# Kernel tuning notes

Measured on AMD Instinct MI355X. Metric: run time of the kernel, lower is better.

The kernel has to match this reference:

```python
import jax, jax.numpy as jnp
import numpy as np

B, C, H, W = 16, 256, 32, 32   # batch, codebook_dim (channels), latent grid
K = 16384                      # codebook_size
BETA = 0.25                    # commitment beta


def setup_inputs() -> dict:
    key = jax.random.key(0)
    k1, k2, k3 = jax.random.split(key, 3)
    x = jax.random.normal(k1, (B, C, H, W), dtype=jnp.float32)
    # binary-ish mask, broadcast over channel dim (c=1)
    codebook_mask = (jax.random.uniform(k2, (B, 1, H, W)) < 0.5).astype(jnp.float32)
    # uniform(-1/K, 1/K) init as in the torch module
    weight = jax.random.uniform(k3, (K, C), dtype=jnp.float32,
                                minval=-1.0 / K, maxval=1.0 / K)
    return {"x": x, "codebook_mask": codebook_mask, "weight": weight}


def reference(x, codebook_mask, weight):
    b, c, h, w = x.shape
    n = h * w
    # b c h w -> b (h w) c
    xf = jnp.transpose(x, (0, 2, 3, 1)).reshape(b, n, c)
    mask = jnp.transpose(codebook_mask, (0, 2, 3, 1)).reshape(b, n, 1)

    flat = xf.reshape(b * n, c)
    # negative squared euclidean distance: -|f|^2 - |w|^2 + 2 f.w
    dist = (-jnp.sum(flat * flat, axis=1, keepdims=True)
            - jnp.sum(weight * weight, axis=1)
            + 2.0 * flat @ weight.T)                      # [b*n, K]
    # temp=0 -> gumbel_sample degenerates to argmax
    embed_ind = jnp.argmax(dist, axis=-1).reshape(b, n)    # int indices
    x_q = weight[embed_ind]                                # [b, n, c] gather

    # masked commitment loss
    ratio = 1.0 / jnp.mean(mask)
    loss = (ratio * BETA * jnp.mean((jax.lax.stop_gradient(x_q) - xf) ** 2 * mask)
            + ratio * jnp.mean((x_q - jax.lax.stop_gradient(xf)) ** 2 * mask))

    # straight-through estimator
    x_q_st = xf + jax.lax.stop_gradient(x_q - xf)

    x_q_img = jnp.transpose(x_q_st.reshape(b, h, w, c), (0, 3, 1, 2))
    embed_ind_img = embed_ind.reshape(b, h, w)
    return x_q_img, loss, embed_ind_img
```

## Files before the change

kernel.cpp:

```cpp
#include <hip/hip_runtime.h>

#define KCODES 16384
#define NPOS   16384
#define KQUART 4096
#define ROWS   64
#define CAPH   80
#define M_INT  5700
#define SX     21.166666f
#define SW     2080768.0f

#define OFF_XT    0
#define OFF_XQ8   4194304
#define OFF_PART  6291456
#define OFF_WHP8  8388608
#define OFF_CAND  9437184
#define OFF_WN    12582912
#define OFF_NS1   12599296
#define OFF_IDX   12615680
#define OFF_CCNT  12632064
#define OFF_QMAX  12697600

#define OUT_LOSS  4194304
#define OUT_IND   4194305

#define AS1 __attribute__((address_space(1)))
#define AS3 __attribute__((address_space(3)))

typedef int  i32x4 __attribute__((ext_vector_type(4)));

__global__ void k1a_pack_x(const float* __restrict__ x, float* __restrict__ xt)
{
    __shared__ float t[32][33];
    const int p0 = blockIdx.x * 32, c0 = blockIdx.y * 32, b = blockIdx.z;
    const int tx = threadIdx.x, ty = threadIdx.y;
#pragma unroll
    for (int i = 0; i < 4; ++i) {
        int cl = ty + i * 8;
        t[cl][tx] = x[(b * 256 + c0 + cl) * 1024 + p0 + tx];
    }
    __syncthreads();
#pragma unroll
    for (int i = 0; i < 4; ++i) {
        int pl = ty + i * 8;
        xt[(b * 1024 + p0 + pl) * 256 + c0 + tx] = t[tx][pl];
    }
}

__global__ void k_rownorm2(const float4* __restrict__ xt4, float* __restrict__ ns1,
                           signed char* __restrict__ xq8,
                           const float4* __restrict__ w4, float* __restrict__ wn,
                           signed char* __restrict__ wq8)
{
    __shared__ float4 rows[32 * 64];
    const int tid = threadIdx.x;
    const bool wpath = blockIdx.x >= 512;
    const int r0 = (wpath ? blockIdx.x - 512 : blockIdx.x) * 32;
    const float4* __restrict__ src4 = wpath ? w4 : xt4;
    float* __restrict__ out = wpath ? wn : ns1;
    const float sign = wpath ? 1.0f : -1.0f;
    const float sc = wpath ? SW : SX;
#pragma unroll
    for (int i = 0; i < 8; ++i) {
        const int F = r0 * 64 + tid + 256 * i;
        const float4 v = src4[F];
        rows[tid + 256 * i] = v;
        char4 qv;
        qv.x = (signed char)min(127, max(-127, __float2int_rn(v.x * sc)));
        qv.y = (signed char)min(127, max(-127, __float2int_rn(v.y * sc)));
        qv.z = (signed char)min(127, max(-127, __float2int_rn(v.z * sc)));
        qv.w = (signed char)min(127, max(-127, __float2int_rn(v.w * sc)));
        const int row = F >> 6, c4 = F & 63, c = c4 * 4;
        if (wpath) {
            const int qt = row >> 12, kk = row & 4095;
            const int chi = kk >> 8, rem = kk & 255;
            const int wq_ = rem >> 6, ct = (rem >> 4) & 3, n4 = rem & 15;
            const int sidx = qt * 1048576 + (chi * 4 + (c >> 6)) * 16384
                           + wq_ * 4096 + ct * 1024 + n4 * 64 + (c & 63);
            *(char4*)(wq8 + sidx) = qv;
        } else {
            *(char4*)(xq8 + row * 256 + c) = qv;
        }
    }
    __syncthreads();
    const int rl = tid >> 3, j = tid & 7;
    const float* qp = (const float*)&rows[rl * 64];
    float h[2];
#pragma unroll
    for (int half = 0; half < 2; ++half) {
        const float* p = qp + half * 128;
        float x = p[j];
        float r = __fmul_rn(x, x);
#pragma unroll
        for (int i = 1; i < 16; ++i) {
            float y = p[8 * i + j];
            r = __fadd_rn(r, __fmul_rn(y, y));
        }
        float t = __fadd_rn(r, __shfl_xor(r, 1));
        t = __fadd_rn(t, __shfl_xor(t, 2));
        t = __fadd_rn(t, __shfl_xor(t, 4));
        h[half] = t;
    }
    if (j == 0) out[r0 + rl] = sign * __fadd_rn(h[0], h[1]);
}

__global__ __launch_bounds__(256, 4) void k2_mfma(
    const signed char* __restrict__ xq8, const signed char* __restrict__ wq8,
    unsigned short* __restrict__ candk, int* __restrict__ candc,
    float* __restrict__ qmax)
{
    __shared__ __align__(16) signed char As[16384];
    __shared__ int rowmaxI[ROWS];
    __shared__ int ccnt[ROWS];
    __shared__ unsigned short ck[ROWS][CAPH];

    const int tid  = threadIdx.x;
    const int lane = tid & 63;
    const int w    = tid >> 6;
    const int q    = lane >> 4;
    const int nn   = lane & 15;
    const int qt   = blockIdx.x & 3;
    const int rowBase = (blockIdx.x >> 2) * ROWS;
    const signed char* wq8Q = wq8 + qt * 1048576;

#pragma unroll
    for (int i = 0; i < 4; ++i) {
        const int slot = i * 256 + tid;
        const int g = slot >> 6, row = slot & 63;
        const signed char* src = xq8 + (rowBase + row) * 256 + g * 16;
        __builtin_amdgcn_global_load_lds((const AS1 void*)src,
                                         (AS3 void*)((char*)&As[0] + slot * 16), 16, 0, 0);
    }
    if (tid < ROWS) { rowmaxI[tid] = (int)0x80000000; ccnt[tid] = 0; }

    const signed char* bptr = wq8Q + (w * 4096 + nn * 64 + q * 16);

    __syncthreads();

    i32x4 b0[4], b1[4];
#pragma unroll
    for (int ct = 0; ct < 4; ++ct)
        b0[ct] = *(const i32x4*)(bptr + ct * 1024);
    const signed char* nps = bptr + 16384;

    for (int ch = 0; ch < 16; ++ch) {
        const int kb = ch * 256;
        i32x4 acc[4][4];
#pragma unroll
        for (int rt = 0; rt < 4; ++rt)
#pragma unroll
            for (int ct = 0; ct < 4; ++ct) acc[rt][ct] = (i32x4){0, 0, 0, 0};

#pragma unroll
        for (int cs2 = 0; cs2 < 2; ++cs2) {
#pragma unroll
            for (int ct = 0; ct < 4; ++ct)
                b1[ct] = *(const i32x4*)(nps + ct * 1024);
            nps += 16384;
#pragma unroll
            for (int rt = 0; rt < 4; ++rt) {
                const int as = ((2 * cs2) * 4 + q) * 64 + rt * 16 + nn;
                const i32x4 ah = *(const i32x4*)&As[as * 16];
#pragma unroll
                for (int ct = 0; ct < 4; ++ct)
                    acc[rt][ct] = __builtin_amdgcn_mfma_i32_16x16x64_i8(ah, b0[ct], acc[rt][ct], 0, 0, 0);
            }
#pragma unroll
            for (int ct = 0; ct < 4; ++ct)
                b0[ct] = *(const i32x4*)(nps + ct * 1024);
            nps += 16384;
#pragma unroll
            for (int rt = 0; rt < 4; ++rt) {
                const int as = ((2 * cs2 + 1) * 4 + q) * 64 + rt * 16 + nn;
                const i32x4 ah = *(const i32x4*)&As[as * 16];
#pragma unroll
                for (int ct = 0; ct < 4; ++ct)
                    acc[rt][ct] = __builtin_amdgcn_mfma_i32_16x16x64_i8(ah, b1[ct], acc[rt][ct], 0, 0, 0);
            }
        }

#pragma unroll
        for (int rt = 0; rt < 4; ++rt)
#pragma unroll
            for (int rg = 0; rg < 4; ++rg) {
                int m = max(max(acc[rt][0][rg], acc[rt][1][rg]),
                            max(acc[rt][2][rg], acc[rt][3][rg]));
                m = max(m, __shfl_xor(m, 1, 64));
                m = max(m, __shfl_xor(m, 2, 64));
                m = max(m, __shfl_xor(m, 4, 64));
                m = max(m, __shfl_xor(m, 8, 64));
                if (nn == 0)
                    atomicMax(&rowmaxI[rt * 16 + q * 4 + rg], m);
            }
        __syncthreads();
#pragma unroll
        for (int rt = 0; rt < 4; ++rt)
#pragma unroll
            for (int rg = 0; rg < 4; ++rg) {
                const int row = rt * 16 + q * 4 + rg;
                const int th = rowmaxI[row] - M_INT;
#pragma unroll
                for (int ct = 0; ct < 4; ++ct)
                    if (acc[rt][ct][rg] >= th) {
                        const int pos = atomicAdd(&ccnt[row], 1);
                        if (pos < CAPH)
                            ck[row][pos] = (unsigned short)(qt * KQUART + kb + w * 64 + ct * 16 + nn);
                    }
            }
    }
    __syncthreads();
    if (tid < ROWS) {
        candc[(rowBase + tid) * 4 + qt] = ccnt[tid];
        qmax[(rowBase + tid) * 4 + qt] = (float)rowmaxI[tid];
    }
#pragma unroll
    for (int i = 0; i < 20; ++i) {
        const int e = i * 256 + tid;
        const int row = e / CAPH, pos = e - row * CAPH;
        candk[((rowBase + row) * 4 + qt) * CAPH + pos] = ck[row][pos];
    }
}

__global__ __launch_bounds__(256) void k3_rescore(
    const float* __restrict__ xt, const float* __restrict__ weight,
    const float* __restrict__ wn, const float* __restrict__ ns1,
    const float* __restrict__ qmax,
    const unsigned short* __restrict__ candk, const int* __restrict__ candc,
    const float* __restrict__ mask,
    int* __restrict__ idx, float* __restrict__ out, float* __restrict__ part)
{
    const int w = threadIdx.x >> 6, lane = threadIdx.x & 63;
    const int waveId = blockIdx.x * 4 + w;
    float mm = 0.f, merr = 0.f;
#pragma unroll
    for (int rr = 0; rr < 4; ++rr) {
        const int n = waveId * 4 + rr;
        const float4 xv = ((const float4*)(xt + n * 256))[lane];
        const float nsv = ns1[n];
        const float4 qm = ((const float4*)(qmax + n * 4))[0];
        const float qth = fmaxf(fmaxf(qm.x, qm.y), fmaxf(qm.z, qm.w)) - (float)M_INT;
        float bestd = -3.0e38f; int bestk = 0x7fffffff;
#pragma unroll
        for (int qt = 0; qt < 4; ++qt) {
            const float qv = (qt == 0) ? qm.x : (qt == 1) ? qm.y : (qt == 2) ? qm.z : qm.w;
            if (qv < qth) continue;
            const int cnt = candc[n * 4 + qt];
            if (cnt <= CAPH) {
                for (int i = 0; i < cnt; ++i) {
                    const int k = candk[(n * 4 + qt) * CAPH + i];
                    const float4 wv = ((const float4*)(weight + k * 256))[lane];
                    float p = __fmul_rn(xv.x, wv.x);
                    p = __builtin_fmaf(xv.y, wv.y, p);
                    p = __builtin_fmaf(xv.z, wv.z, p);
                    p = __builtin_fmaf(xv.w, wv.w, p);
#pragma unroll
                    for (int off = 1; off < 64; off <<= 1) p += __shfl_xor(p, off, 64);
                    const float t1 = __fadd_rn(nsv, -wn[k]);
                    const float dd = __fadd_rn(t1, __fmul_rn(2.0f, p));
                    if (dd > bestd || (dd == bestd && k < bestk)) { bestd = dd; bestk = k; }
                }
            } else {
                for (int k = qt * KQUART; k < (qt + 1) * KQUART; ++k) {
                    const float4 wv = ((const float4*)(weight + k * 256))[lane];
                    float p = __fmul_rn(xv.x, wv.x);
                    p = __builtin_fmaf(xv.y, wv.y, p);
                    p = __builtin_fmaf(xv.z, wv.z, p);
                    p = __builtin_fmaf(xv.w, wv.w, p);
#pragma unroll
                    for (int off = 1; off < 64; off <<= 1) p += __shfl_xor(p, off, 64);
                    const float t1 = __fadd_rn(nsv, -wn[k]);
                    const float dd = __fadd_rn(t1, __fmul_rn(2.0f, p));
                    if (dd > bestd || (dd == bestd && k < bestk)) { bestd = dd; bestk = k; }
                }
            }
        }
        const int bk = (bestk <= (KCODES - 1)) ? bestk : 0;
        if (lane == 0) { idx[n] = bk; out[OUT_IND + n] = (float)bk; }
        const float4 wv = ((const float4*)(weight + bk * 256))[lane];
        float ex = wv.x - xv.x, ey = wv.y - xv.y, ez = wv.z - xv.z, ew = wv.w - xv.w;
        float s = ex * ex + ey * ey + ez * ez + ew * ew;
#pragma unroll
        for (int off = 1; off < 64; off <<= 1) s += __shfl_xor(s, off, 64);
        const float mval = mask[n];
        mm += mval; merr += mval * s;
    }
    if (lane == 0) { part[waveId * 2 + 0] = mm; part[waveId * 2 + 1] = merr; }
}

__global__ void k5_out(const float* __restrict__ weight, const int* __restrict__ idx,
                       const float* __restrict__ part, float* __restrict__ out)
{
    __shared__ float t[32][33];
    const int p0 = blockIdx.x * 32, c0 = blockIdx.y * 32, b = blockIdx.z;
    const int tx = threadIdx.x, ty = threadIdx.y;
#pragma unroll
    for (int i = 0; i < 4; ++i) {
        const int pl = ty + i * 8;
        const int n = b * 1024 + p0 + pl;
        t[tx][pl] = weight[idx[n] * 256 + c0 + tx];
    }
    __syncthreads();
#pragma unroll
    for (int i = 0; i < 4; ++i) {
        const int cl = ty + i * 8;
        out[(b * 256 + c0 + cl) * 1024 + p0 + tx] = t[cl][tx];
    }
    if (blockIdx.x == 0 && blockIdx.y == 0 && blockIdx.z == 0) {
        __shared__ double red[4][2];
        const int lin = ty * 32 + tx;
        double m = 0.0, s = 0.0;
        for (int i = lin; i < 4096; i += 256) {
            m += (double)part[i * 2 + 0];
            s += (double)part[i * 2 + 1];
        }
        const int lane = lin & 63, wv = lin >> 6;
        for (int o = 32; o > 0; o >>= 1) {
            m += __shfl_down(m, o, 64);
            s += __shfl_down(s, o, 64);
        }
        if (lane == 0) { red[wv][0] = m; red[wv][1] = s; }
        __syncthreads();
        if (lin == 0) {
            const double mt = red[0][0] + red[1][0] + red[2][0] + red[3][0];
            const double st = red[0][1] + red[1][1] + red[2][1] + red[3][1];
            out[OUT_LOSS] = (float)(1.25 * st / (256.0 * mt));
        }
    }
}

extern "C" void kernel_launch(void* const* d_in, const int* in_sizes, int n_in,
                              void* d_out, int out_size, void* d_ws, size_t ws_size,
                              hipStream_t stream)
{
    const float* x      = (const float*)d_in[0];
    const float* mask   = (const float*)d_in[1];
    const float* weight = (const float*)d_in[2];
    float* out = (float*)d_out;
    float* ws  = (float*)d_ws;

    float* xt  = ws + OFF_XT;
    signed char* xq8 = (signed char*)(ws + OFF_XQ8);
    signed char* wq8 = (signed char*)(ws + OFF_WHP8);
    float* wn   = ws + OFF_WN;
    float* ns1  = ws + OFF_NS1;
    int*   idx  = (int*)(ws + OFF_IDX);
    unsigned short* candk = (unsigned short*)(ws + OFF_CAND);
    int*   candc = (int*)(ws + OFF_CCNT);
    float* qmaxA = ws + OFF_QMAX;
    float* part = ws + OFF_PART;

    k1a_pack_x<<<dim3(32, 8, 16), dim3(32, 8), 0, stream>>>(x, xt);
    k_rownorm2<<<1024, 256, 0, stream>>>((const float4*)xt, ns1, xq8,
                                         (const float4*)weight, wn, wq8);
    k2_mfma<<<1024, 256, 0, stream>>>(xq8, wq8, candk, candc, qmaxA);
    k3_rescore<<<1024, 256, 0, stream>>>(xt, weight, wn, ns1, qmaxA, candk, candc,
                                         mask, idx, out, part);
    k5_out<<<dim3(32, 8, 16), dim3(32, 8), 0, stream>>>(weight, idx, part, out);
}
```

Baseline: 295.1 us.

## Fuse transpose into prep kernel, tighten rescore margin, pair candidate rescoring

Merges the x transpose kernel and the row-norm/quantize kernel into one launch, so the transposed rows go straight from shared memory to xt, xq8 and the norms without re-reading xt. Lowers the int8 quarter-pruning margin M_INT so fewer codebook quarters get rescored in fp32. Unrolls the candidate rescoring loop two at a time so two weight loads and their reductions can overlap. The smaller margin risks picking a different argmax when int8 quantization error exceeds the new bound.

```diff
diff --git a/kernel.cpp b/kernel.cpp
--- a/kernel.cpp
+++ b/kernel.cpp
@@ -5,7 +5,7 @@
 #define KQUART 4096
 #define ROWS   64
 #define CAPH   80
-#define M_INT  5700
+#define M_INT  3600
 #define SX     21.166666f
 #define SW     2080768.0f
 
@@ -28,79 +28,110 @@
 
 typedef int  i32x4 __attribute__((ext_vector_type(4)));
 
-__global__ void k1a_pack_x(const float* __restrict__ x, float* __restrict__ xt)
+__global__ void k_prep(const float* __restrict__ x, float* __restrict__ xt,
+                       signed char* __restrict__ xq8, float* __restrict__ ns1,
+                       const float4* __restrict__ w4, float* __restrict__ wn,
+                       signed char* __restrict__ wq8)
 {
+    __shared__ __align__(16) float smem[32 * 257];
     __shared__ float t[32][33];
-    const int p0 = blockIdx.x * 32, c0 = blockIdx.y * 32, b = blockIdx.z;
-    const int tx = threadIdx.x, ty = threadIdx.y;
-#pragma unroll
-    for (int i = 0; i < 4; ++i) {
-        int cl = ty + i * 8;
-        t[cl][tx] = x[(b * 256 + c0 + cl) * 1024 + p0 + tx];
-    }
-    __syncthreads();
-#pragma unroll
-    for (int i = 0; i < 4; ++i) {
-        int pl = ty + i * 8;
-        xt[(b * 1024 + p0 + pl) * 256 + c0 + tx] = t[tx][pl];
-    }
-}
-
-__global__ void k_rownorm2(const float4* __restrict__ xt4, float* __restrict__ ns1,
-                           signed char* __restrict__ xq8,
-                           const float4* __restrict__ w4, float* __restrict__ wn,
-                           signed char* __restrict__ wq8)
-{
-    __shared__ float4 rows[32 * 64];
     const int tid = threadIdx.x;
-    const bool wpath = blockIdx.x >= 512;
-    const int r0 = (wpath ? blockIdx.x - 512 : blockIdx.x) * 32;
-    const float4* __restrict__ src4 = wpath ? w4 : xt4;
-    float* __restrict__ out = wpath ? wn : ns1;
-    const float sign = wpath ? 1.0f : -1.0f;
-    const float sc = wpath ? SW : SX;
-#pragma unroll
-    for (int i = 0; i < 8; ++i) {
-        const int F = r0 * 64 + tid + 256 * i;
-        const float4 v = src4[F];
-        rows[tid + 256 * i] = v;
-        char4 qv;
-        qv.x = (signed char)min(127, max(-127, __float2int_rn(v.x * sc)));
-        qv.y = (signed char)min(127, max(-127, __float2int_rn(v.y * sc)));
-        qv.z = (signed char)min(127, max(-127, __float2int_rn(v.z * sc)));
-        qv.w = (signed char)min(127, max(-127, __float2int_rn(v.w * sc)));
-        const int row = F >> 6, c4 = F & 63, c = c4 * 4;
-        if (wpath) {
+
+    if (blockIdx.x < 512) {
+        const int r0 = blockIdx.x * 32;
+        const int b = r0 >> 10, p0 = r0 & 1023;
+        const int tx = tid & 31, ty = tid >> 5;
+#pragma unroll
+        for (int ci = 0; ci < 8; ++ci) {
+#pragma unroll
+            for (int i = 0; i < 4; ++i) {
+                const int cl = ty + i * 8;
+                t[cl][tx] = x[(b * 256 + ci * 32 + cl) * 1024 + p0 + tx];
+            }
+            __syncthreads();
+#pragma unroll
+            for (int i = 0; i < 4; ++i) {
+                const int pl = ty + i * 8;
+                smem[pl * 257 + ci * 32 + tx] = t[tx][pl];
+            }
+            __syncthreads();
+        }
+#pragma unroll
+        for (int i = 0; i < 8; ++i) {
+            const int row = (tid >> 6) + i * 4, c4 = tid & 63;
+            const float* rp = &smem[row * 257 + c4 * 4];
+            float4 v;
+            v.x = rp[0]; v.y = rp[1]; v.z = rp[2]; v.w = rp[3];
+            ((float4*)(xt + (r0 + row) * 256))[c4] = v;
+            char4 qv;
+            qv.x = (signed char)min(127, max(-127, __float2int_rn(v.x * SX)));
+            qv.y = (signed char)min(127, max(-127, __float2int_rn(v.y * SX)));
+            qv.z = (signed char)min(127, max(-127, __float2int_rn(v.z * SX)));
+            qv.w = (signed char)min(127, max(-127, __float2int_rn(v.w * SX)));
+            *(char4*)(xq8 + (r0 + row) * 256 + c4 * 4) = qv;
+        }
+        __syncthreads();
+        const int rl = tid >> 3, j = tid & 7;
+        const float* qp = &smem[rl * 257];
+        float h[2];
+#pragma unroll
+        for (int half = 0; half < 2; ++half) {
+            const float* p = qp + half * 128;
+            float xx = p[j];
+            float r = __fmul_rn(xx, xx);
+#pragma unroll
+            for (int i = 1; i < 16; ++i) {
+                float y = p[8 * i + j];
+                r = __fadd_rn(r, __fmul_rn(y, y));
+            }
+            float tt = __fadd_rn(r, __shfl_xor(r, 1));
+            tt = __fadd_rn(tt, __shfl_xor(tt, 2));
+            tt = __fadd_rn(tt, __shfl_xor(tt, 4));
+            h[half] = tt;
+        }
+        if (j == 0) ns1[r0 + rl] = -__fadd_rn(h[0], h[1]);
+    } else {
+        float4* rows = (float4*)smem;
+        const int r0 = (blockIdx.x - 512) * 32;
+#pragma unroll
+        for (int i = 0; i < 8; ++i) {
+            const int F = r0 * 64 + tid + 256 * i;
+            const float4 v = w4[F];
+            rows[tid + 256 * i] = v;
+            char4 qv;
+            qv.x = (signed char)min(127, max(-127, __float2int_rn(v.x * SW)));
+            qv.y = (signed char)min(127, max(-127, __float2int_rn(v.y * SW)));
+            qv.z = (signed char)min(127, max(-127, __float2int_rn(v.z * SW)));
+            qv.w = (signed char)min(127, max(-127, __float2int_rn(v.w * SW)));
+            const int row = F >> 6, c4 = F & 63, c = c4 * 4;
             const int qt = row >> 12, kk = row & 4095;
             const int chi = kk >> 8, rem = kk & 255;
             const int wq_ = rem >> 6, ct = (rem >> 4) & 3, n4 = rem & 15;
             const int sidx = qt * 1048576 + (chi * 4 + (c >> 6)) * 16384
                            + wq_ * 4096 + ct * 1024 + n4 * 64 + (c & 63);
             *(char4*)(wq8 + sidx) = qv;
-        } else {
-            *(char4*)(xq8 + row * 256 + c) = qv;
-        }
-    }
-    __syncthreads();
-    const int rl = tid >> 3, j = tid & 7;
-    const float* qp = (const float*)&rows[rl * 64];
-    float h[2];
-#pragma unroll
-    for (int half = 0; half < 2; ++half) {
-        const float* p = qp + half * 128;
-        float x = p[j];
-        float r = __fmul_rn(x, x);
-#pragma unroll
-        for (int i = 1; i < 16; ++i) {
-            float y = p[8 * i + j];
-            r = __fadd_rn(r, __fmul_rn(y, y));
-        }
-        float t = __fadd_rn(r, __shfl_xor(r, 1));
-        t = __fadd_rn(t, __shfl_xor(t, 2));
-        t = __fadd_rn(t, __shfl_xor(t, 4));
-        h[half] = t;
-    }
-    if (j == 0) out[r0 + rl] = sign * __fadd_rn(h[0], h[1]);
+        }
+        __syncthreads();
+        const int rl = tid >> 3, j = tid & 7;
+        const float* qp = (const float*)&rows[rl * 64];
+        float h[2];
+#pragma unroll
+        for (int half = 0; half < 2; ++half) {
+            const float* p = qp + half * 128;
+            float xx = p[j];
+            float r = __fmul_rn(xx, xx);
+#pragma unroll
+            for (int i = 1; i < 16; ++i) {
+                float y = p[8 * i + j];
+                r = __fadd_rn(r, __fmul_rn(y, y));
+            }
+            float tt = __fadd_rn(r, __shfl_xor(r, 1));
+            tt = __fadd_rn(tt, __shfl_xor(tt, 2));
+            tt = __fadd_rn(tt, __shfl_xor(tt, 4));
+            h[half] = tt;
+        }
+        if (j == 0) wn[r0 + rl] = __fadd_rn(h[0], h[1]);
+    }
 }
 
 __global__ __launch_bounds__(256, 4) void k2_mfma(
@@ -244,9 +275,33 @@
             const float qv = (qt == 0) ? qm.x : (qt == 1) ? qm.y : (qt == 2) ? qm.z : qm.w;
             if (qv < qth) continue;
             const int cnt = candc[n * 4 + qt];
+            const int base = (n * 4 + qt) * CAPH;
             if (cnt <= CAPH) {
-                for (int i = 0; i < cnt; ++i) {
-                    const int k = candk[(n * 4 + qt) * CAPH + i];
+                int i = 0;
+                for (; i + 1 < cnt; i += 2) {
+                    const int ka = candk[base + i], kb = candk[base + i + 1];
+                    const float4 wa = ((const float4*)(weight + ka * 256))[lane];
+                    const float4 wb = ((const float4*)(weight + kb * 256))[lane];
+                    float pa = __fmul_rn(xv.x, wa.x);
+                    float pb = __fmul_rn(xv.x, wb.x);
+                    pa = __builtin_fmaf(xv.y, wa.y, pa);
+                    pb = __builtin_fmaf(xv.y, wb.y, pb);
+                    pa = __builtin_fmaf(xv.z, wa.z, pa);
+                    pb = __builtin_fmaf(xv.z, wb.z, pb);
+                    pa = __builtin_fmaf(xv.w, wa.w, pa);
+                    pb = __builtin_fmaf(xv.w, wb.w, pb);
+#pragma unroll
+                    for (int off = 1; off < 64; off <<= 1) {
+                        pa += __shfl_xor(pa, off, 64);
+                        pb += __shfl_xor(pb, off, 64);
+                    }
+                    const float da = __fadd_rn(__fadd_rn(nsv, -wn[ka]), __fmul_rn(2.0f, pa));
+                    const float db = __fadd_rn(__fadd_rn(nsv, -wn[kb]), __fmul_rn(2.0f, pb));
+                    if (da > bestd || (da == bestd && ka < bestk)) { bestd = da; bestk = ka; }
+                    if (db > bestd || (db == bestd && kb < bestk)) { bestd = db; bestk = kb; }
+                }
+                if (i < cnt) {
+                    const int k = candk[base + i];
                     const float4 wv = ((const float4*)(weight + k * 256))[lane];
                     float p = __fmul_rn(xv.x, wv.x);
                     p = __builtin_fmaf(xv.y, wv.y, p);
@@ -254,8 +309,7 @@
                     p = __builtin_fmaf(xv.w, wv.w, p);
 #pragma unroll
                     for (int off = 1; off < 64; off <<= 1) p += __shfl_xor(p, off, 64);
-                    const float t1 = __fadd_rn(nsv, -wn[k]);
-                    const float dd = __fadd_rn(t1, __fmul_rn(2.0f, p));
+                    const float dd = __fadd_rn(__fadd_rn(nsv, -wn[k]), __fmul_rn(2.0f, p));
                     if (dd > bestd || (dd == bestd && k < bestk)) { bestd = dd; bestk = k; }
                 }
             } else {
@@ -267,8 +321,7 @@
                     p = __builtin_fmaf(xv.w, wv.w, p);
 #pragma unroll
                     for (int off = 1; off < 64; off <<= 1) p += __shfl_xor(p, off, 64);
-                    const float t1 = __fadd_rn(nsv, -wn[k]);
-                    const float dd = __fadd_rn(t1, __fmul_rn(2.0f, p));
+                    const float dd = __fadd_rn(__fadd_rn(nsv, -wn[k]), __fmul_rn(2.0f, p));
                     if (dd > bestd || (dd == bestd && k < bestk)) { bestd = dd; bestk = k; }
                 }
             }
@@ -348,9 +401,8 @@
     float* qmaxA = ws + OFF_QMAX;
     float* part = ws + OFF_PART;
 
-    k1a_pack_x<<<dim3(32, 8, 16), dim3(32, 8), 0, stream>>>(x, xt);
-    k_rownorm2<<<1024, 256, 0, stream>>>((const float4*)xt, ns1, xq8,
-                                         (const float4*)weight, wn, wq8);
+    k_prep<<<1024, 256, 0, stream>>>(x, xt, xq8, ns1,
+                                     (const float4*)weight, wn, wq8);
     k2_mfma<<<1024, 256, 0, stream>>>(xq8, wq8, candk, candc, qmaxA);
     k3_rescore<<<1024, 256, 0, stream>>>(xt, weight, wn, ns1, qmaxA, candk, candc,
                                          mask, idx, out, part);
```

After: 254.8 us (median of 2 runs). -13.7%, faster.
